# Performance work log

Measured on AMD Instinct MI355X. Metric: run time of the kernel, lower is better.

## Reference

```python
import jax, jax.numpy as jnp
import numpy as np

N_NODES = 100000
K_NBRS = 16
N_EDGES = N_NODES * K_NBRS


def setup_inputs() -> dict:
    key = jax.random.key(0)
    ks = jax.random.split(key, 20)
    x = jax.random.normal(ks[0], (N_NODES, 3), dtype=jnp.float32)
    # knn-like edge list: every node is the target of exactly K_NBRS edges
    dst = jnp.repeat(jnp.arange(N_NODES, dtype=jnp.int64), K_NBRS)
    src = jax.random.randint(ks[1], (N_EDGES,), 0, N_NODES, dtype=jnp.int64)
    edge_index = jnp.stack([src, dst], axis=0)  # [2, E], row0=source(j), row1=target(i)

    def lin_init(k, fan_in, fan_out):
        s = 1.0 / np.sqrt(fan_in)
        return jax.random.uniform(k, (fan_in, fan_out), jnp.float32, -s, s)

    inp = {"x": x, "edge_index": edge_index}
    inp["W1"], inp["b1"] = lin_init(ks[2], 6, 64), jnp.zeros((64,), jnp.float32)
    for i, kk in zip(range(2, 6), ks[3:7]):
        inp[f"W{i}"] = lin_init(kk, 128, 64)
        inp[f"b{i}"] = jnp.zeros((64,), jnp.float32)
    inp["Wa"], inp["ba"] = lin_init(ks[8], 128, 128), jnp.zeros((128,), jnp.float32)
    inp["Wb"], inp["bb"] = lin_init(ks[9], 128, 3), jnp.zeros((3,), jnp.float32)
    return inp


def edge_conv(x, src, dst, W, b):
    # PyG EdgeConv: message = nn(cat([x_i, x_j - x_i])), max-aggregate at target i
    xi = x[dst]                      # [E, C] center (target) features
    xj = x[src]                      # [E, C] neighbor (source) features
    msg = jnp.concatenate([xi, xj - xi], axis=-1)  # [E, 2C]
    msg = jax.nn.relu(msg @ W + b)                 # [E, 64] per-edge MLP
    return jax.ops.segment_max(msg, dst, num_segments=N_NODES)  # [N, 64]


def reference(x, edge_index, W1, b1, W2, b2, W3, b3, W4, b4, W5, b5, Wa, ba, Wb, bb):
    src, dst = edge_index[0], edge_index[1]
    h = edge_conv(x, src, dst, W1, b1)
    h = edge_conv(h, src, dst, W2, b2)
    h = edge_conv(h, src, dst, W3, b3)
    h = edge_conv(h, src, dst, W4, b4)
    h = edge_conv(h, src, dst, W5, b5)           # [N, 64]
    g = jnp.max(h, axis=0, keepdims=True)        # [1, 64] global max
    feat = jnp.concatenate([h, jnp.broadcast_to(g, h.shape)], axis=1)  # [N, 128]
    out = jax.nn.relu(feat @ Wa + ba) @ Wb + bb  # [N, 3]
    return x + out
```

## Files before the change

kernel.cpp:

```cpp
#include <hip/hip_runtime.h>
#include <math.h>

#define N_NODES 100000
#define K_NBRS 16
#define N_EDGES (N_NODES * K_NBRS)
#define TPB 256
#define NBLK 2048

typedef __attribute__((ext_vector_type(8))) short short8;
typedef __attribute__((ext_vector_type(8))) float float8;
typedef __attribute__((ext_vector_type(4))) float float4_;

__device__ __forceinline__ unsigned short f2bf(float f) {
  unsigned int u = __float_as_uint(f);
  u += 0x7fffu + ((u >> 16) & 1u);
  return (unsigned short)(u >> 16);
}
__device__ __forceinline__ float bf2f(unsigned short b) {
  return __uint_as_float(((unsigned int)b) << 16);
}

__global__ void k_normsrc(const int* __restrict__ ei, int* __restrict__ srcout) {
  const bool is64 = (ei[1] == 0) && (ei[3] == 0) && (ei[5] == 0) && (ei[7] == 0);
  const int tid = blockIdx.x * blockDim.x + threadIdx.x;
  const int stride = gridDim.x * blockDim.x;
  for (int e = tid; e < N_EDGES; e += stride)
    srcout[e] = is64 ? ei[2 * e] : ei[e];
}

__global__ void k_layer1(const float* __restrict__ x, const float* __restrict__ W1,
                         const float* __restrict__ b1,
                         float* __restrict__ A, unsigned short* __restrict__ B) {
  const int lane = threadIdx.x & 63;
  const int nwaves = (gridDim.x * blockDim.x) >> 6;
  const int wid0 = (blockIdx.x * blockDim.x + threadIdx.x) >> 6;
  float w[6];
#pragma unroll
  for (int k = 0; k < 6; ++k) w[k] = W1[k * 64 + lane];
  const float bias = b1[lane];
  for (int i0 = wid0; i0 < N_NODES; i0 += nwaves) {
    const int i = __builtin_amdgcn_readfirstlane(i0);
    const float x0 = x[3 * i], x1 = x[3 * i + 1], x2 = x[3 * i + 2];
    const float b = fmaf(x0, w[3], fmaf(x1, w[4], x2 * w[5]));
    const float a = bias + fmaf(x0, w[0] - w[3],
                          fmaf(x1, w[1] - w[4], x2 * (w[2] - w[5])));
    A[(size_t)i * 64 + lane] = a;
    B[(size_t)i * 64 + lane] = f2bf(b);
  }
}

template <bool DO_GMAX>
__global__ void k_aggr(const int* __restrict__ src,
                       const float* __restrict__ Ain,
                       const unsigned short* __restrict__ Bin,
                       float* __restrict__ hout, float* __restrict__ P) {
  const int lane = threadIdx.x & 63;
  const int nw = (gridDim.x * blockDim.x) >> 6;
  const int w0 = (blockIdx.x * blockDim.x + threadIdx.x) >> 6;
  float gm = 0.f;
  for (int p = w0; p * 2 < N_NODES; p += nw) {
    const int i = __builtin_amdgcn_readfirstlane(p * 2);
    const int* sp = src + (size_t)i * K_NBRS;
    unsigned short gv[32];
#pragma unroll
    for (int e = 0; e < 32; ++e)
      gv[e] = Bin[(size_t)sp[e] * 64 + lane];
    const float a0 = Ain[(size_t)i * 64 + lane];
    const float a1 = Ain[(size_t)(i + 1) * 64 + lane];
    float m0 = 0.f, m1 = 0.f;
#pragma unroll
    for (int e = 0; e < 16; ++e) m0 = fmaxf(m0, a0 + bf2f(gv[e]));
#pragma unroll
    for (int e = 0; e < 16; ++e) m1 = fmaxf(m1, a1 + bf2f(gv[16 + e]));
    hout[(size_t)i * 64 + lane] = m0;
    hout[(size_t)(i + 1) * 64 + lane] = m1;
    if constexpr (DO_GMAX) gm = fmaxf(gm, fmaxf(m0, m1));
  }
  if constexpr (DO_GMAX) {
    __shared__ float red[TPB];
    red[threadIdx.x] = gm;
    __syncthreads();
    if (threadIdx.x < 64) {
      P[(size_t)blockIdx.x * 64 + threadIdx.x] =
          fmaxf(fmaxf(red[threadIdx.x], red[threadIdx.x + 64]),
                fmaxf(red[threadIdx.x + 128], red[threadIdx.x + 192]));
    }
  }
}

__global__ __launch_bounds__(TPB, 2)
void k_gemm(const float* __restrict__ h, const float* __restrict__ W,
            const float* __restrict__ bn,
            float* __restrict__ Aout, unsigned short* __restrict__ Bout) {
  __shared__ unsigned short lwhi[128 * 72];
  __shared__ unsigned short lwlo[128 * 72];
  for (int idx = threadIdx.x; idx < 8192; idx += TPB) {
    const int k = idx >> 7, j = idx & 127;
    const float v = (j < 64) ? (W[k * 64 + j] - W[(64 + k) * 64 + j])
                             : W[(64 + k) * 64 + (j - 64)];
    const unsigned short hi = f2bf(v);
    lwhi[j * 72 + k] = hi;
    lwlo[j * 72 + k] = f2bf(v - bf2f(hi));
  }
  __syncthreads();
  const int lane = threadIdx.x & 63;
  const int wav = threadIdx.x >> 6;
  const int l15 = lane & 15, lg = lane >> 4;
  short8 bhi[8][2], blo[8][2];
#pragma unroll
  for (int ct = 0; ct < 8; ++ct)
#pragma unroll
    for (int kk = 0; kk < 2; ++kk) {
      const int off = (ct * 16 + l15) * 72 + kk * 32 + lg * 8;
      bhi[ct][kk] = *(const short8*)&lwhi[off];
      blo[ct][kk] = *(const short8*)&lwlo[off];
    }
  float bv[4];
#pragma unroll
  for (int ct = 0; ct < 4; ++ct) bv[ct] = bn[ct * 16 + l15];
  const int NT = (N_NODES + 63) / 64;
  for (int t = blockIdx.x; t < NT; t += gridDim.x) {
    const int nb = t * 64 + wav * 16;
    const int row = min(nb + l15, N_NODES - 1);
    const float* hr = h + (size_t)row * 64;
    float4_ acc[8];
#pragma unroll
    for (int ct = 0; ct < 8; ++ct) acc[ct] = (float4_)(0.f);
#pragma unroll
    for (int kk = 0; kk < 2; ++kk) {
      const float8 hv = *(const float8*)(hr + kk * 32 + lg * 8);
      short8 ahi, alo;
#pragma unroll
      for (int e = 0; e < 8; ++e) {
        const unsigned short hb = f2bf(hv[e]);
        ahi[e] = (short)hb;
        alo[e] = (short)f2bf(hv[e] - bf2f(hb));
      }
#pragma unroll
      for (int ct = 0; ct < 8; ++ct) {
        acc[ct] = __builtin_amdgcn_mfma_f32_16x16x32_bf16(ahi, bhi[ct][kk], acc[ct], 0, 0, 0);
        acc[ct] = __builtin_amdgcn_mfma_f32_16x16x32_bf16(alo, bhi[ct][kk], acc[ct], 0, 0, 0);
        acc[ct] = __builtin_amdgcn_mfma_f32_16x16x32_bf16(ahi, blo[ct][kk], acc[ct], 0, 0, 0);
      }
    }
#pragma unroll
    for (int ct = 0; ct < 8; ++ct)
#pragma unroll
      for (int r = 0; r < 4; ++r) {
        const int node = nb + lg * 4 + r;
        if (node < N_NODES) {
          if (ct < 4)
            Aout[(size_t)node * 64 + ct * 16 + l15] = acc[ct][r] + bv[ct];
          else
            Bout[(size_t)node * 64 + (ct - 4) * 16 + l15] = f2bf(acc[ct][r]);
        }
      }
  }
}

__global__ void k_gred(const float* __restrict__ P, float* __restrict__ g) {
  __shared__ float red[16][64];
  const int lane = threadIdx.x & 63;
  const int w = threadIdx.x >> 6;
  float m = 0.f;
  for (int r = w; r < NBLK; r += 16)
    m = fmaxf(m, P[(size_t)r * 64 + lane]);
  red[w][lane] = m;
  __syncthreads();
  if (threadIdx.x < 64) {
    float mm = 0.f;
#pragma unroll
    for (int k = 0; k < 16; ++k) mm = fmaxf(mm, red[k][lane]);
    g[lane] = mm;
  }
}

__global__ __launch_bounds__(TPB, 2)
void k_final(const float* __restrict__ h, const float* __restrict__ g,
             const float* __restrict__ Wa, const float* __restrict__ ba,
             const float* __restrict__ Wb, const float* __restrict__ bb,
             const float* __restrict__ x, float* __restrict__ out) {
  __shared__ unsigned short lwhi[128 * 72];
  __shared__ unsigned short lwlo[128 * 72];
  __shared__ float sgt[128];
  for (int idx = threadIdx.x; idx < 8192; idx += TPB) {
    const int k = idx >> 7, j = idx & 127;
    const float v = Wa[k * 128 + j];
    const unsigned short hi = f2bf(v);
    lwhi[j * 72 + k] = hi;
    lwlo[j * 72 + k] = f2bf(v - bf2f(hi));
  }
  if (threadIdx.x < 128) {
    const int c = threadIdx.x;
    float s = ba[c];
    for (int k = 0; k < 64; ++k) s = fmaf(g[k], Wa[(64 + k) * 128 + c], s);
    sgt[c] = s;
  }
  __syncthreads();
  const int lane = threadIdx.x & 63;
  const int wav = threadIdx.x >> 6;
  const int l15 = lane & 15, lg = lane >> 4;
  short8 bhi[8][2], blo[8][2];
#pragma unroll
  for (int ct = 0; ct < 8; ++ct)
#pragma unroll
    for (int kk = 0; kk < 2; ++kk) {
      const int off = (ct * 16 + l15) * 72 + kk * 32 + lg * 8;
      bhi[ct][kk] = *(const short8*)&lwhi[off];
      blo[ct][kk] = *(const short8*)&lwlo[off];
    }
  float gtv[8];
#pragma unroll
  for (int ct = 0; ct < 8; ++ct) gtv[ct] = sgt[ct * 16 + l15];
  float wbv[8][3];
#pragma unroll
  for (int ct = 0; ct < 8; ++ct)
#pragma unroll
    for (int jj = 0; jj < 3; ++jj)
      wbv[ct][jj] = Wb[(ct * 16 + l15) * 3 + jj];
  const float bbl = (l15 == 0) ? bb[0] : (l15 == 1 ? bb[1] : bb[2]);
  const int NT = (N_NODES + 63) / 64;
  for (int t = blockIdx.x; t < NT; t += gridDim.x) {
    const int nb = t * 64 + wav * 16;
    const int row = min(nb + l15, N_NODES - 1);
    const float* hr = h + (size_t)row * 64;
    float4_ acc[8];
#pragma unroll
    for (int ct = 0; ct < 8; ++ct) acc[ct] = (float4_)(0.f);
#pragma unroll
    for (int kk = 0; kk < 2; ++kk) {
      const float8 hv = *(const float8*)(hr + kk * 32 + lg * 8);
      short8 ahi, alo;
#pragma unroll
      for (int e = 0; e < 8; ++e) {
        const unsigned short hb = f2bf(hv[e]);
        ahi[e] = (short)hb;
        alo[e] = (short)f2bf(hv[e] - bf2f(hb));
      }
#pragma unroll
      for (int ct = 0; ct < 8; ++ct) {
        acc[ct] = __builtin_amdgcn_mfma_f32_16x16x32_bf16(ahi, bhi[ct][kk], acc[ct], 0, 0, 0);
        acc[ct] = __builtin_amdgcn_mfma_f32_16x16x32_bf16(alo, bhi[ct][kk], acc[ct], 0, 0, 0);
        acc[ct] = __builtin_amdgcn_mfma_f32_16x16x32_bf16(ahi, blo[ct][kk], acc[ct], 0, 0, 0);
      }
    }
#pragma unroll
    for (int r = 0; r < 4; ++r) {
      float t0 = 0.f, t1 = 0.f, t2 = 0.f;
#pragma unroll
      for (int ct = 0; ct < 8; ++ct) {
        const float hd = fmaxf(acc[ct][r] + gtv[ct], 0.f);
        t0 = fmaf(hd, wbv[ct][0], t0);
        t1 = fmaf(hd, wbv[ct][1], t1);
        t2 = fmaf(hd, wbv[ct][2], t2);
      }
#pragma unroll
      for (int off = 1; off < 16; off <<= 1) {
        t0 += __shfl_xor(t0, off);
        t1 += __shfl_xor(t1, off);
        t2 += __shfl_xor(t2, off);
      }
      const int node = nb + lg * 4 + r;
      if (node < N_NODES && l15 < 3) {
        const float tj = (l15 == 0) ? t0 : (l15 == 1 ? t1 : t2);
        out[(size_t)node * 3 + l15] = x[(size_t)node * 3 + l15] + tj + bbl;
      }
    }
  }
}

extern "C" void kernel_launch(void* const* d_in, const int* in_sizes, int n_in,
                              void* d_out, int out_size, void* d_ws, size_t ws_size,
                              hipStream_t stream) {
  const float* x  = (const float*)d_in[0];
  const int*   ei = (const int*)d_in[1];
  const float* W1 = (const float*)d_in[2];
  const float* b1 = (const float*)d_in[3];
  const float* W2 = (const float*)d_in[4];
  const float* b2 = (const float*)d_in[5];
  const float* W3 = (const float*)d_in[6];
  const float* b3 = (const float*)d_in[7];
  const float* W4 = (const float*)d_in[8];
  const float* b4 = (const float*)d_in[9];
  const float* W5 = (const float*)d_in[10];
  const float* b5 = (const float*)d_in[11];
  const float* Wa = (const float*)d_in[12];
  const float* ba = (const float*)d_in[13];
  const float* Wb = (const float*)d_in[14];
  const float* bb = (const float*)d_in[15];
  float* out = (float*)d_out;

  float* ws = (float*)d_ws;
  int* srcbuf = (int*)ws;
  float* A0 = ws + 1600000;
  float* A1 = A0 + 6400000;
  float* H  = A1 + 6400000;
  unsigned short* B0 = (unsigned short*)(H + 6400000);
  unsigned short* B1 = B0 + 6400000;
  float* P = (float*)(B1 + 6400000);
  float* g = P + (size_t)NBLK * 64;

  k_normsrc<<<1024, TPB, 0, stream>>>(ei, srcbuf);
  k_layer1<<<NBLK, TPB, 0, stream>>>(x, W1, b1, A0, B0);
  k_aggr<false><<<NBLK, TPB, 0, stream>>>(srcbuf, A0, B0, H, nullptr);
  k_gemm<<<512, TPB, 0, stream>>>(H, W2, b2, A1, B1);
  k_aggr<false><<<NBLK, TPB, 0, stream>>>(srcbuf, A1, B1, H, nullptr);
  k_gemm<<<512, TPB, 0, stream>>>(H, W3, b3, A0, B0);
  k_aggr<false><<<NBLK, TPB, 0, stream>>>(srcbuf, A0, B0, H, nullptr);
  k_gemm<<<512, TPB, 0, stream>>>(H, W4, b4, A1, B1);
  k_aggr<false><<<NBLK, TPB, 0, stream>>>(srcbuf, A1, B1, H, nullptr);
  k_gemm<<<512, TPB, 0, stream>>>(H, W5, b5, A0, B0);
  k_aggr<true><<<NBLK, TPB, 0, stream>>>(srcbuf, A0, B0, H, P);
  k_gred<<<1, 1024, 0, stream>>>(P, g);
  k_final<<<512, TPB, 0, stream>>>(H, g, Wa, ba, Wb, bb, x, out);
}
```

Before: 419.8 us.

## Store aggregated features as bf16 and vectorize neighbor gather across lane groups

The aggregation kernel now has each wave process four nodes. Each lane loads four contiguous bf16 channels per neighbor with vector loads, and the quarter-wave partial maxima are combined with cross-lane shuffles. It adds the centre term after the neighbor max, which is algebraically equivalent. The aggregated hidden features are written as bf16 instead of fp32, so the GEMM and final kernels read half the bytes and skip the split-precision conversion and one of the three MFMAs per tile. This lowers memory traffic and instruction count, at the cost of rounding intermediate activations to bf16, which may affect accuracy.

```diff
diff --git a/kernel.cpp b/kernel.cpp
--- a/kernel.cpp
+++ b/kernel.cpp
@@ -10,6 +10,8 @@
 typedef __attribute__((ext_vector_type(8))) short short8;
 typedef __attribute__((ext_vector_type(8))) float float8;
 typedef __attribute__((ext_vector_type(4))) float float4_;
+typedef __attribute__((ext_vector_type(4))) int int4_;
+typedef __attribute__((ext_vector_type(4))) unsigned short ushort4_;
 
 __device__ __forceinline__ unsigned short f2bf(float f) {
   unsigned int u = __float_as_uint(f);
@@ -53,43 +55,76 @@
 __global__ void k_aggr(const int* __restrict__ src,
                        const float* __restrict__ Ain,
                        const unsigned short* __restrict__ Bin,
-                       float* __restrict__ hout, float* __restrict__ P) {
-  const int lane = threadIdx.x & 63;
+                       unsigned short* __restrict__ hout, float* __restrict__ P) {
+  const int lane = threadIdx.x & 63;
+  const int q = lane >> 4;
+  const int c4 = (lane & 15) * 4;
   const int nw = (gridDim.x * blockDim.x) >> 6;
   const int w0 = (blockIdx.x * blockDim.x + threadIdx.x) >> 6;
-  float gm = 0.f;
-  for (int p = w0; p * 2 < N_NODES; p += nw) {
-    const int i = __builtin_amdgcn_readfirstlane(p * 2);
-    const int* sp = src + (size_t)i * K_NBRS;
-    unsigned short gv[32];
-#pragma unroll
-    for (int e = 0; e < 32; ++e)
-      gv[e] = Bin[(size_t)sp[e] * 64 + lane];
-    const float a0 = Ain[(size_t)i * 64 + lane];
-    const float a1 = Ain[(size_t)(i + 1) * 64 + lane];
-    float m0 = 0.f, m1 = 0.f;
-#pragma unroll
-    for (int e = 0; e < 16; ++e) m0 = fmaxf(m0, a0 + bf2f(gv[e]));
-#pragma unroll
-    for (int e = 0; e < 16; ++e) m1 = fmaxf(m1, a1 + bf2f(gv[16 + e]));
-    hout[(size_t)i * 64 + lane] = m0;
-    hout[(size_t)(i + 1) * 64 + lane] = m1;
-    if constexpr (DO_GMAX) gm = fmaxf(gm, fmaxf(m0, m1));
+  float4_ gmax = (float4_)(0.f);
+  for (int p = w0; p * 4 < N_NODES; p += nw) {
+    const int i0 = __builtin_amdgcn_readfirstlane(p * 4);
+    int4_ idx[4];
+#pragma unroll
+    for (int n = 0; n < 4; ++n)
+      idx[n] = *(const int4_*)(src + (size_t)(i0 + n) * 16 + q * 4);
+    ushort4_ gv[4][4];
+#pragma unroll
+    for (int n = 0; n < 4; ++n)
+#pragma unroll
+      for (int e = 0; e < 4; ++e)
+        gv[n][e] = *(const ushort4_*)(Bin + (size_t)idx[n][e] * 64 + c4);
+    const float4_ av = *(const float4_*)(Ain + (size_t)(i0 + q) * 64 + c4);
+    float4_ m[4];
+#pragma unroll
+    for (int n = 0; n < 4; ++n) {
+#pragma unroll
+      for (int t = 0; t < 4; ++t) {
+        const float v0 = bf2f(gv[n][0][t]), v1 = bf2f(gv[n][1][t]);
+        const float v2 = bf2f(gv[n][2][t]), v3 = bf2f(gv[n][3][t]);
+        m[n][t] = fmaxf(fmaxf(v0, v1), fmaxf(v2, v3));
+      }
+#pragma unroll
+      for (int t = 0; t < 4; ++t) {
+        float v = m[n][t];
+        v = fmaxf(v, __shfl_xor(v, 16));
+        v = fmaxf(v, __shfl_xor(v, 32));
+        m[n][t] = v;
+      }
+    }
+    ushort4_ hb;
+#pragma unroll
+    for (int t = 0; t < 4; ++t) {
+      float v = m[0][t];
+      v = (q == 1) ? m[1][t] : v;
+      v = (q == 2) ? m[2][t] : v;
+      v = (q == 3) ? m[3][t] : v;
+      const float h = fmaxf(av[t] + v, 0.f);
+      hb[t] = f2bf(h);
+      if constexpr (DO_GMAX) gmax[t] = fmaxf(gmax[t], h);
+    }
+    *(ushort4_*)(hout + (size_t)(i0 + q) * 64 + c4) = hb;
   }
   if constexpr (DO_GMAX) {
-    __shared__ float red[TPB];
-    red[threadIdx.x] = gm;
+    __shared__ float red[TPB][4];
+#pragma unroll
+    for (int t = 0; t < 4; ++t) red[threadIdx.x][t] = gmax[t];
     __syncthreads();
     if (threadIdx.x < 64) {
-      P[(size_t)blockIdx.x * 64 + threadIdx.x] =
-          fmaxf(fmaxf(red[threadIdx.x], red[threadIdx.x + 64]),
-                fmaxf(red[threadIdx.x + 128], red[threadIdx.x + 192]));
+      const int c = threadIdx.x, j = c >> 2, t = c & 3;
+      float mm = 0.f;
+#pragma unroll
+      for (int w = 0; w < 4; ++w)
+#pragma unroll
+        for (int qq = 0; qq < 4; ++qq)
+          mm = fmaxf(mm, red[w * 64 + qq * 16 + j][t]);
+      P[(size_t)blockIdx.x * 64 + c] = mm;
     }
   }
 }
 
 __global__ __launch_bounds__(TPB, 2)
-void k_gemm(const float* __restrict__ h, const float* __restrict__ W,
+void k_gemm(const unsigned short* __restrict__ h, const float* __restrict__ W,
             const float* __restrict__ bn,
             float* __restrict__ Aout, unsigned short* __restrict__ Bout) {
   __shared__ unsigned short lwhi[128 * 72];
@@ -122,24 +157,16 @@
   for (int t = blockIdx.x; t < NT; t += gridDim.x) {
     const int nb = t * 64 + wav * 16;
     const int row = min(nb + l15, N_NODES - 1);
-    const float* hr = h + (size_t)row * 64;
+    const unsigned short* hr = h + (size_t)row * 64;
     float4_ acc[8];
 #pragma unroll
     for (int ct = 0; ct < 8; ++ct) acc[ct] = (float4_)(0.f);
 #pragma unroll
     for (int kk = 0; kk < 2; ++kk) {
-      const float8 hv = *(const float8*)(hr + kk * 32 + lg * 8);
-      short8 ahi, alo;
-#pragma unroll
-      for (int e = 0; e < 8; ++e) {
-        const unsigned short hb = f2bf(hv[e]);
-        ahi[e] = (short)hb;
-        alo[e] = (short)f2bf(hv[e] - bf2f(hb));
-      }
+      const short8 ahi = *(const short8*)(hr + kk * 32 + lg * 8);
 #pragma unroll
       for (int ct = 0; ct < 8; ++ct) {
         acc[ct] = __builtin_amdgcn_mfma_f32_16x16x32_bf16(ahi, bhi[ct][kk], acc[ct], 0, 0, 0);
-        acc[ct] = __builtin_amdgcn_mfma_f32_16x16x32_bf16(alo, bhi[ct][kk], acc[ct], 0, 0, 0);
         acc[ct] = __builtin_amdgcn_mfma_f32_16x16x32_bf16(ahi, blo[ct][kk], acc[ct], 0, 0, 0);
       }
     }
@@ -176,7 +203,7 @@
 }
 
 __global__ __launch_bounds__(TPB, 2)
-void k_final(const float* __restrict__ h, const float* __restrict__ g,
+void k_final(const unsigned short* __restrict__ h, const float* __restrict__ g,
              const float* __restrict__ Wa, const float* __restrict__ ba,
              const float* __restrict__ Wb, const float* __restrict__ bb,
              const float* __restrict__ x, float* __restrict__ out) {
@@ -223,24 +250,16 @@
   for (int t = blockIdx.x; t < NT; t += gridDim.x) {
     const int nb = t * 64 + wav * 16;
     const int row = min(nb + l15, N_NODES - 1);
-    const float* hr = h + (size_t)row * 64;
+    const unsigned short* hr = h + (size_t)row * 64;
     float4_ acc[8];
 #pragma unroll
     for (int ct = 0; ct < 8; ++ct) acc[ct] = (float4_)(0.f);
 #pragma unroll
     for (int kk = 0; kk < 2; ++kk) {
-      const float8 hv = *(const float8*)(hr + kk * 32 + lg * 8);
-      short8 ahi, alo;
-#pragma unroll
-      for (int e = 0; e < 8; ++e) {
-        const unsigned short hb = f2bf(hv[e]);
-        ahi[e] = (short)hb;
-        alo[e] = (short)f2bf(hv[e] - bf2f(hb));
-      }
+      const short8 ahi = *(const short8*)(hr + kk * 32 + lg * 8);
 #pragma unroll
       for (int ct = 0; ct < 8; ++ct) {
         acc[ct] = __builtin_amdgcn_mfma_f32_16x16x32_bf16(ahi, bhi[ct][kk], acc[ct], 0, 0, 0);
-        acc[ct] = __builtin_amdgcn_mfma_f32_16x16x32_bf16(alo, bhi[ct][kk], acc[ct], 0, 0, 0);
         acc[ct] = __builtin_amdgcn_mfma_f32_16x16x32_bf16(ahi, blo[ct][kk], acc[ct], 0, 0, 0);
       }
     }
@@ -294,8 +313,8 @@
   int* srcbuf = (int*)ws;
   float* A0 = ws + 1600000;
   float* A1 = A0 + 6400000;
-  float* H  = A1 + 6400000;
-  unsigned short* B0 = (unsigned short*)(H + 6400000);
+  unsigned short* H  = (unsigned short*)(A1 + 6400000);
+  unsigned short* B0 = H + 6400000;
   unsigned short* B1 = B0 + 6400000;
   float* P = (float*)(B1 + 6400000);
   float* g = P + (size_t)NBLK * 64;
```

Result: faster. 378.5 us (-9.8%).
